# Performance work log

Measured on AMD Instinct MI355X. Metric: run time of the kernel, lower is better.

Reference implementation:

```python
import jax, jax.numpy as jnp
import numpy as np

H = 16        # query heads
HK = 8        # key/value heads
HD = 128      # head dim
EPS = 1e-6
THETA = 1000000.0


def _rmsnorm(x, w):
    # per-head RMSNorm over last dim (head_dim)
    var = jnp.mean(jnp.square(x.astype(jnp.float32)), axis=-1, keepdims=True)
    return (x * jax.lax.rsqrt(var + EPS)).astype(x.dtype) * w


def _rope(x, cos, sin):
    # x: [B, S, h, HD]; cos/sin: [S, HD//2]
    x1, x2 = jnp.split(x, 2, axis=-1)
    c = cos[None, :, None, :]
    s = sin[None, :, None, :]
    return jnp.concatenate([x1 * c - x2 * s, x2 * c + x1 * s], axis=-1)


def setup_inputs() -> dict:
    key = jax.random.key(0)
    ks = jax.random.split(key, 5)
    B, S, D = 2, 2048, 2048
    scale = 0.02
    return {
        "x": jax.random.normal(ks[0], (B, S, D), jnp.float32),
        "wq": jax.random.normal(ks[1], (H * HD, D), jnp.float32) * scale,
        "wk": jax.random.normal(ks[2], (HK * HD, D), jnp.float32) * scale,
        "wv": jax.random.normal(ks[3], (HK * HD, D), jnp.float32) * scale,
        "wo": jax.random.normal(ks[4], (D, H * HD), jnp.float32) * scale,
        "q_norm_w": jnp.ones((HD,), jnp.float32),
        "k_norm_w": jnp.ones((HD,), jnp.float32),
    }


def reference(x, wq, wk, wv, wo, q_norm_w, k_norm_w):
    B, S, D = x.shape
    # QKV projections (no bias)
    q = (x @ wq.T).reshape(B, S, H, HD)
    k = (x @ wk.T).reshape(B, S, HK, HD)
    v = (x @ wv.T).reshape(B, S, HK, HD)

    # per-head RMSNorm on Q and K (Qwen3 qk-norm)
    q = _rmsnorm(q, q_norm_w)
    k = _rmsnorm(k, k_norm_w)

    # RoPE
    inv_freq = 1.0 / (THETA ** (jnp.arange(0, HD, 2, dtype=jnp.float32) / HD))
    ang = jnp.arange(S, dtype=jnp.float32)[:, None] * inv_freq[None, :]  # [S, HD/2]
    cos, sin = jnp.cos(ang), jnp.sin(ang)
    q = _rope(q, cos, sin)
    k = _rope(k, cos, sin)

    # GQA: repeat KV heads to match query heads
    rep = H // HK
    k = jnp.repeat(k, rep, axis=2)  # [B, S, H, HD]
    v = jnp.repeat(v, rep, axis=2)

    # causal SDPA
    scores = jnp.einsum("bqhd,bkhd->bhqk", q, k) / jnp.sqrt(jnp.float32(HD))
    mask = jnp.tril(jnp.ones((S, S), dtype=bool))
    scores = jnp.where(mask[None, None], scores, jnp.finfo(scores.dtype).min)
    probs = jax.nn.softmax(scores, axis=-1)
    out = jnp.einsum("bhqk,bkhd->bqhd", probs, v).reshape(B, S, H * HD)

    return out @ wo.T
```

## Files before the change

kernel.cpp:

```cpp
#include <hip/hip_runtime.h>
#include <hip/hip_bf16.h>
#include <math.h>

#define B_   2
#define S_   2048
#define D_   2048
#define H_   16
#define HK_  8
#define HD_  128
#define BS_  (B_ * S_)
#define NQKV 4096
#define SCALE 0.08838834764831845f

typedef __bf16 bf16x8 __attribute__((ext_vector_type(8)));
typedef __bf16 bf16x4 __attribute__((ext_vector_type(4)));
typedef float  f32x4  __attribute__((ext_vector_type(4)));

#define AS1(p) ((const __attribute__((address_space(1))) void*)(p))
#define AS3(p) ((__attribute__((address_space(3))) void*)(p))

template <int S>
__device__ __forceinline__ float ror16(float x) {
    return __builtin_bit_cast(float, __builtin_amdgcn_update_dpp(
        0, __builtin_bit_cast(int, x), 0x120 | S, 0xF, 0xF, true));
}
__device__ __forceinline__ float row_sum16(float x) {
    x += ror16<8>(x);
    x += ror16<4>(x);
    x += ror16<2>(x);
    x += ror16<1>(x);
    return x;
}

__global__ __launch_bounds__(256) void cvt_all(const float* __restrict__ x,
                                               const float* __restrict__ wq,
                                               const float* __restrict__ wk,
                                               const float* __restrict__ wv,
                                               const float* __restrict__ wo,
                                               __bf16* __restrict__ xb,
                                               __bf16* __restrict__ wb,
                                               __bf16* __restrict__ wob) {
    int bid = blockIdx.x;
    const float* src;
    __bf16* dst;
    int i4;
    if (bid < 8192)       { src = x;  dst = xb;                    i4 = bid * 256; }
    else if (bid < 12288) { src = wq; dst = wb;                    i4 = (bid - 8192) * 256; }
    else if (bid < 14336) { src = wk; dst = wb + (size_t)4194304;  i4 = (bid - 12288) * 256; }
    else if (bid < 16384) { src = wv; dst = wb + (size_t)6291456;  i4 = (bid - 14336) * 256; }
    else                  { src = wo; dst = wob;                   i4 = (bid - 16384) * 256; }
    i4 += threadIdx.x;
    float4 v = reinterpret_cast<const float4*>(src)[i4];
    bf16x4 o = {(__bf16)v.x, (__bf16)v.y, (__bf16)v.z, (__bf16)v.w};
    reinterpret_cast<bf16x4*>(dst)[i4] = o;
}

__global__ __launch_bounds__(128) void build_rope(float* __restrict__ tab) {
    int s = blockIdx.x;
    int d = threadIdx.x;
    int i = d & 63;
    float inv_freq = exp2f(-19.931568569324174f * (float)(2 * i) * (1.0f / 128.0f));
    float ang = (float)s * inv_freq;
    float sn, cs;
    sincosf(ang, &sn, &cs);
    tab[s * 128 + d] = (d < 64) ? cs : sn;
}

__global__ __launch_bounds__(512, 2) void gemm_bf16_8ph(const __bf16* __restrict__ A,
                                                        const __bf16* __restrict__ W,
                                                        __bf16* __restrict__ C,
                                                        int M, int N, int K) {
    __shared__ __bf16 lds[2][2][256 * 64];

    const int t    = threadIdx.x;
    const int w    = t >> 6;
    const int lane = t & 63;
    const int col  = lane & 15;
    const int quad = lane >> 4;
    const int c7   = col & 7;
    const int wm   = w >> 2;
    const int wn   = w & 3;

    const int bid = blockIdx.x;
    const int nid = (bid & 7) * 32 + (bid >> 3);
    const int st  = nid >> 4;
    const int wi  = nid & 15;
    const int m0 = ((st >> 2) * 4 + (wi >> 2)) * 256;
    const int n0 = ((st & 3) * 4 + (wi & 3)) * 256;

    const int lr8 = lane >> 3;
    const int sw8 = ((lane & 7) ^ lr8) * 8;
    const __bf16* Ag = A + (size_t)(m0 + w * 16 + lr8) * K + sw8;
    const __bf16* Wg = W + (size_t)(n0 + w * 16 + lr8) * K + sw8;

    const int nkt = K >> 6;
    const int nit = nkt >> 1;

    const int aBase = (wm * 128 + col) * 64;
    const int bBase = (wn * 64 + col) * 64;
    const int kx0 = (quad ^ c7) * 8;
    const int kx1 = ((4 + quad) ^ c7) * 8;

    f32x4 acc[8][4];
    #pragma unroll
    for (int i = 0; i < 8; i++)
        #pragma unroll
        for (int j = 0; j < 4; j++) acc[i][j] = (f32x4){0.f, 0.f, 0.f, 0.f};

    bf16x8 a[4][2], a2[4][2], b0f[2][2], b1f[2][2];

    auto stg = [&](int ktv, int bufc, int ab, int half) {
        if (ktv >= nkt) return;
        const __bf16* gb = (ab ? Wg : Ag) + (size_t)half * 128 * K + (size_t)ktv * 64;
        __bf16* db = &lds[bufc][ab][(half * 128 + w * 16) * 64];
        __builtin_amdgcn_global_load_lds(AS1(gb), AS3(db), 16, 0, 0);
        __builtin_amdgcn_global_load_lds(AS1(gb + (size_t)8 * K), AS3(db + 512), 16, 0, 0);
    };
    auto lda = [&](bf16x8 (&dst)[4][2], const __bf16* panel, int g) {
        #pragma unroll
        for (int mi = 0; mi < 4; mi++) {
            dst[mi][0] = *reinterpret_cast<const bf16x8*>(&panel[aBase + (g * 64 + mi * 16) * 64 + kx0]);
            dst[mi][1] = *reinterpret_cast<const bf16x8*>(&panel[aBase + (g * 64 + mi * 16) * 64 + kx1]);
        }
    };
    auto ldb = [&](bf16x8 (&dst)[2][2], const __bf16* panel, int ng) {
        #pragma unroll
        for (int ni = 0; ni < 2; ni++) {
            dst[ni][0] = *reinterpret_cast<const bf16x8*>(&panel[bBase + (ng * 32 + ni * 16) * 64 + kx0]);
            dst[ni][1] = *reinterpret_cast<const bf16x8*>(&panel[bBase + (ng * 32 + ni * 16) * 64 + kx1]);
        }
    };
    auto mm = [&](bf16x8 (&af)[4][2], bf16x8 (&bfr)[2][2], int g, int ng) {
        __builtin_amdgcn_s_setprio(1);
        #pragma unroll
        for (int mi = 0; mi < 4; mi++)
            #pragma unroll
            for (int ni = 0; ni < 2; ni++) {
                f32x4 c = acc[g * 4 + mi][ng * 2 + ni];
                c = __builtin_amdgcn_mfma_f32_16x16x32_bf16(af[mi][0], bfr[ni][0], c, 0, 0, 0);
                c = __builtin_amdgcn_mfma_f32_16x16x32_bf16(af[mi][1], bfr[ni][1], c, 0, 0, 0);
                acc[g * 4 + mi][ng * 2 + ni] = c;
            }
        __builtin_amdgcn_s_setprio(0);
    };

#define BAR  __builtin_amdgcn_s_barrier()
#define LGKM0 do { asm volatile("s_waitcnt lgkmcnt(0)" ::: "memory"); \
                   __builtin_amdgcn_sched_barrier(0); } while (0)
#define VM(n) asm volatile("s_waitcnt vmcnt(" #n ")" ::: "memory")

    stg(0, 0, 0, 0); stg(0, 0, 0, 1); stg(0, 0, 1, 0); stg(0, 0, 1, 1);
    stg(1, 1, 0, 0); stg(1, 1, 0, 1);
    VM(4);
    BAR;

    #pragma unroll 1
    for (int it = 0; it < nit; ++it) {
        const int k2 = it * 2;
        const bool last = (it == nit - 1);

        const __bf16* A0p = &lds[0][0][0];
        const __bf16* B0p = &lds[0][1][0];
        const __bf16* A1p = &lds[1][0][0];
        const __bf16* B1p = &lds[1][1][0];

        lda(a, A0p, 0); ldb(b0f, B0p, 0);
        stg(k2 + 1, 1, 1, 0);
        BAR; LGKM0;
        mm(a, b0f, 0, 0);
        lda(a2, A0p, 1);
        stg(k2 + 1, 1, 1, 1);
        BAR; LGKM0;
        mm(a2, b0f, 1, 0);
        ldb(b1f, B0p, 1);
        stg(k2 + 2, 0, 0, 0);
        BAR; LGKM0;
        mm(a, b1f, 0, 1);
        stg(k2 + 2, 0, 0, 1);
        if (last) VM(0); else VM(4);
        BAR;
        mm(a2, b1f, 1, 1);

        lda(a, A1p, 0); ldb(b0f, B1p, 0);
        stg(k2 + 2, 0, 1, 0);
        BAR; LGKM0;
        mm(a, b0f, 0, 0);
        lda(a2, A1p, 1);
        stg(k2 + 2, 0, 1, 1);
        BAR; LGKM0;
        mm(a2, b0f, 1, 0);
        ldb(b1f, B1p, 1);
        stg(k2 + 3, 1, 0, 0);
        BAR; LGKM0;
        mm(a, b1f, 0, 1);
        stg(k2 + 3, 1, 0, 1);
        if (!last) { VM(4); }
        BAR;
        mm(a2, b1f, 1, 1);
    }

#undef BAR
#undef LGKM0
#undef VM

    #pragma unroll
    for (int m8 = 0; m8 < 8; m8++) {
        #pragma unroll
        for (int r = 0; r < 4; r++) {
            size_t row = m0 + wm * 128 + m8 * 16 + quad * 4 + r;
            __bf16* cp = C + row * N + n0 + wn * 64 + col;
            #pragma unroll
            for (int n4 = 0; n4 < 4; n4++) cp[n4 * 16] = (__bf16)acc[m8][n4][r];
        }
    }
}

template <typename CT>
__global__ __launch_bounds__(256) void gemm_bf16_nt(const __bf16* __restrict__ A,
                                                    const __bf16* __restrict__ W,
                                                    CT* __restrict__ C,
                                                    int M, int N, int K) {
    __shared__ __bf16 As[128 * 64];
    __shared__ __bf16 Bs[128 * 64];

    const int t    = threadIdx.x;
    const int w    = t >> 6;
    const int lane = t & 63;
    const int col  = lane & 15;
    const int quad = lane >> 4;
    const int wm   = w >> 1;
    const int wn   = w & 1;

    const int m0 = blockIdx.y * 128;
    const int n0 = blockIdx.x * 128;

    const int lrow8 = lane >> 3;
    const int lch   = ((lane & 7) ^ lrow8) * 8;

    const __bf16* agp = A + (size_t)(m0 + w * 32 + lrow8) * K + lch;
    const __bf16* wgp = W + (size_t)(n0 + w * 32 + lrow8) * K + lch;
    __bf16* alp = As + (w * 32) * 64;
    __bf16* blp = Bs + (w * 32) * 64;

    const int c7 = col & 7;

    f32x4 acc[4][4];
    #pragma unroll
    for (int m = 0; m < 4; m++)
        #pragma unroll
        for (int n = 0; n < 4; n++) acc[m][n] = (f32x4){0.f, 0.f, 0.f, 0.f};

    #pragma unroll 1
    for (int k0 = 0; k0 < K; k0 += 64) {
        #pragma unroll
        for (int j = 0; j < 4; j++) {
            __builtin_amdgcn_global_load_lds(AS1(agp + k0 + (size_t)(j * 8) * K),
                                             AS3(alp + j * 512), 16, 0, 0);
            __builtin_amdgcn_global_load_lds(AS1(wgp + k0 + (size_t)(j * 8) * K),
                                             AS3(blp + j * 512), 16, 0, 0);
        }
        __syncthreads();

        #pragma unroll
        for (int kk = 0; kk < 2; kk++) {
            bf16x8 af[4], bfr[4];
            #pragma unroll
            for (int m = 0; m < 4; m++)
                af[m] = *reinterpret_cast<const bf16x8*>(
                    &As[(wm * 64 + m * 16 + col) * 64 + ((kk * 4 + quad) ^ c7) * 8]);
            #pragma unroll
            for (int n = 0; n < 4; n++)
                bfr[n] = *reinterpret_cast<const bf16x8*>(
                    &Bs[(wn * 64 + n * 16 + col) * 64 + ((kk * 4 + quad) ^ c7) * 8]);

            #pragma unroll
            for (int m = 0; m < 4; m++)
                #pragma unroll
                for (int n = 0; n < 4; n++)
                    acc[m][n] = __builtin_amdgcn_mfma_f32_16x16x32_bf16(af[m], bfr[n], acc[m][n], 0, 0, 0);
        }
        __syncthreads();
    }

    #pragma unroll
    for (int m = 0; m < 4; m++) {
        #pragma unroll
        for (int r = 0; r < 4; r++) {
            size_t row = m0 + wm * 64 + m * 16 + quad * 4 + r;
            CT* cp = C + row * N + n0 + wn * 64 + col;
            #pragma unroll
            for (int n = 0; n < 4; n++) cp[n * 16] = (CT)acc[m][n][r];
        }
    }
}

__global__ __launch_bounds__(256) void norm_rope(__bf16* __restrict__ qkv,
                                                 const float* __restrict__ qw,
                                                 const float* __restrict__ kw,
                                                 const float* __restrict__ tab) {
    const int g    = blockIdx.x * 16 + (threadIdx.x >> 4);
    const int l    = threadIdx.x & 15;
    const int row  = g / 24;
    const int head = g - row * 24;
    const int s    = row & (S_ - 1);

    const float* w = (head < H_) ? qw : kw;
    __bf16* p = qkv + (size_t)row * NQKV + head * HD_ + l * 8;

    bf16x8 xv = *reinterpret_cast<const bf16x8*>(p);
    float xf[8];
    float ss = 0.f;
    #pragma unroll
    for (int j = 0; j < 8; j++) { xf[j] = (float)xv[j]; ss = fmaf(xf[j], xf[j], ss); }
    ss = row_sum16(ss);
    float rs = rsqrtf(ss * (1.0f / 128.0f) + 1e-6f);

    float nf[8];
    const float4 w0 = *reinterpret_cast<const float4*>(&w[l * 8]);
    const float4 w1 = *reinterpret_cast<const float4*>(&w[l * 8 + 4]);
    nf[0] = xf[0] * rs * w0.x; nf[1] = xf[1] * rs * w0.y;
    nf[2] = xf[2] * rs * w0.z; nf[3] = xf[3] * rs * w0.w;
    nf[4] = xf[4] * rs * w1.x; nf[5] = xf[5] * rs * w1.y;
    nf[6] = xf[6] * rs * w1.z; nf[7] = xf[7] * rs * w1.w;

    float of[8];
    #pragma unroll
    for (int j = 0; j < 8; j++) of[j] = __shfl_xor(nf[j], 8);

    const int ib = (l & 7) * 8;
    const float4 c0 = *reinterpret_cast<const float4*>(&tab[s * 128 + ib]);
    const float4 c1 = *reinterpret_cast<const float4*>(&tab[s * 128 + ib + 4]);
    const float4 s0 = *reinterpret_cast<const float4*>(&tab[s * 128 + 64 + ib]);
    const float4 s1 = *reinterpret_cast<const float4*>(&tab[s * 128 + 64 + ib + 4]);
    float cs[8] = {c0.x, c0.y, c0.z, c0.w, c1.x, c1.y, c1.z, c1.w};
    float sn[8] = {s0.x, s0.y, s0.z, s0.w, s1.x, s1.y, s1.z, s1.w};

    bf16x8 out;
    if (l < 8) {
        #pragma unroll
        for (int j = 0; j < 8; j++) out[j] = (__bf16)(nf[j] * cs[j] - of[j] * sn[j]);
    } else {
        #pragma unroll
        for (int j = 0; j < 8; j++) out[j] = (__bf16)(of[j] * sn[j] + nf[j] * cs[j]);
    }
    *reinterpret_cast<bf16x8*>(p) = out;
}

__global__ __launch_bounds__(256) void transpose_v(const __bf16* __restrict__ qkv,
                                                   __bf16* __restrict__ vt) {
    __shared__ __bf16 Ls[64][136];
    const int t  = threadIdx.x;
    const int bk = blockIdx.y;
    const int b  = bk >> 3;
    const int kvh = bk & 7;
    const int s0 = blockIdx.x * 64;

    #pragma unroll
    for (int i = 0; i < 4; i++) {
        int f = t + i * 256;
        int row = f >> 4;
        int d8 = (f & 15) * 8;
        bf16x8 v = *reinterpret_cast<const bf16x8*>(
            &qkv[(size_t)(b * S_ + s0 + row) * NQKV + 3072 + kvh * HD_ + d8]);
        *reinterpret_cast<bf16x8*>(&Ls[row][d8]) = v;
    }
    __syncthreads();

    #pragma unroll
    for (int i = 0; i < 4; i++) {
        int f = t + i * 256;
        int dim = f >> 3;
        int kc = f & 7;
        bf16x8 o;
        #pragma unroll
        for (int e = 0; e < 8; e++) o[e] = Ls[kc * 8 + e][dim];
        *reinterpret_cast<bf16x8*>(
            &vt[((size_t)bk * HD_ + dim) * S_ + s0 + kc * 8]) = o;
    }
}

__global__ __launch_bounds__(256) void attn_mfma(const __bf16* __restrict__ qkv,
                                                 const __bf16* __restrict__ vt,
                                                 __bf16* __restrict__ ao) {
    __shared__ __align__(16) char smem[17408];
    __bf16 (*Qs)[136] = reinterpret_cast<__bf16(*)[136]>(smem);
    __bf16 (*Ks)[136] = reinterpret_cast<__bf16(*)[136]>(smem);
    __shared__ __bf16 Vt[128][72];
    __shared__ __bf16 Ps[4][16][72];

    const int t    = threadIdx.x;
    const int w    = t >> 6;
    const int lane = t & 63;
    const int col  = lane & 15;
    const int quad = lane >> 4;

    const int bh  = blockIdx.x;
    const int b   = bh >> 4;
    const int h   = bh & 15;
    const int kvh = h >> 1;
    const int qb  = gridDim.y - 1 - blockIdx.y;
    const int r0  = qb * 64;

    const float C0 = SCALE * 1.44269504f;
    const float CM = -12.0f * 1.44269504f;

    const __bf16* vbase = vt + ((size_t)(b * HK_ + kvh) * HD_) * S_;

    const __bf16* kp[4];
    __bf16*       kw_[4];
    const __bf16* vp[4];
    __bf16*       vw_[4];
    #pragma unroll
    for (int i = 0; i < 4; i++) {
        int f = t + i * 256;
        int row = f >> 4, d8 = (f & 15) * 8;
        kp[i]  = qkv + (size_t)(b * S_ + row) * NQKV + 2048 + kvh * HD_ + d8;
        kw_[i] = &Ks[row][d8];
        int dim = f >> 3, kc = f & 7;
        vp[i]  = vbase + (size_t)dim * S_ + kc * 8;
        vw_[i] = &Vt[dim][kc * 8];
    }

    bf16x8 kreg[4], vreg[4];
    #pragma unroll
    for (int i = 0; i < 4; i++) {
        kreg[i] = *reinterpret_cast<const bf16x8*>(kp[i]);  kp[i] += (size_t)64 * NQKV;
        vreg[i] = *reinterpret_cast<const bf16x8*>(vp[i]);  vp[i] += 64;
    }

    #pragma unroll
    for (int i = 0; i < 4; i++) {
        int f   = t + i * 256;
        int row = f >> 4;
        int d8  = (f & 15) * 8;
        bf16x8 v = *reinterpret_cast<const bf16x8*>(
            &qkv[(size_t)(b * S_ + r0 + row) * NQKV + h * HD_ + d8]);
        *reinterpret_cast<bf16x8*>(&Qs[row][d8]) = v;
    }
    __syncthreads();

    bf16x8 qf[4];
    {
        const int m = w * 16 + col;
        #pragma unroll
        for (int k = 0; k < 4; k++)
            qf[k] = *reinterpret_cast<const bf16x8*>(&Qs[m][k * 32 + quad * 8]);
    }

    f32x4 o_acc[8];
    #pragma unroll
    for (int i = 0; i < 8; i++) o_acc[i] = (f32x4){0.f, 0.f, 0.f, 0.f};
    float l_lane[4] = {0.f, 0.f, 0.f, 0.f};

    const int ntiles = qb + 1;
    for (int ti = 0; ti < ntiles; ti++) {
        __syncthreads();

        #pragma unroll
        for (int i = 0; i < 4; i++) {
            *reinterpret_cast<bf16x8*>(kw_[i]) = kreg[i];
            *reinterpret_cast<bf16x8*>(vw_[i]) = vreg[i];
        }
        if (ti + 1 < ntiles) {
            #pragma unroll
            for (int i = 0; i < 4; i++) {
                kreg[i] = *reinterpret_cast<const bf16x8*>(kp[i]);  kp[i] += (size_t)64 * NQKV;
                vreg[i] = *reinterpret_cast<const bf16x8*>(vp[i]);  vp[i] += 64;
            }
        }
        __syncthreads();

        f32x4 s[4];
        #pragma unroll
        for (int n = 0; n < 4; n++) {
            f32x4 acc = (f32x4){0.f, 0.f, 0.f, 0.f};
            #pragma unroll
            for (int k = 0; k < 4; k++) {
                bf16x8 bf = *reinterpret_cast<const bf16x8*>(
                    &Ks[n * 16 + col][k * 32 + quad * 8]);
                acc = __builtin_amdgcn_mfma_f32_16x16x32_bf16(qf[k], bf, acc, 0, 0, 0);
            }
            s[n] = acc;
        }

        const bool diag = (ti == qb);
        #pragma unroll
        for (int r = 0; r < 4; r++) {
            float p0 = exp2f(fmaf(s[0][r], C0, CM));
            float p1 = exp2f(fmaf(s[1][r], C0, CM));
            float p2 = exp2f(fmaf(s[2][r], C0, CM));
            float p3 = exp2f(fmaf(s[3][r], C0, CM));
            if (diag) {
                int qloc = w * 16 + quad * 4 + r;
                if (0 * 16 + col > qloc) p0 = 0.f;
                if (1 * 16 + col > qloc) p1 = 0.f;
                if (2 * 16 + col > qloc) p2 = 0.f;
                if (3 * 16 + col > qloc) p3 = 0.f;
            }
            l_lane[r] += p0 + p1 + p2 + p3;
            Ps[w][quad * 4 + r][0 * 16 + col] = (__bf16)p0;
            Ps[w][quad * 4 + r][1 * 16 + col] = (__bf16)p1;
            Ps[w][quad * 4 + r][2 * 16 + col] = (__bf16)p2;
            Ps[w][quad * 4 + r][3 * 16 + col] = (__bf16)p3;
        }

        bf16x8 pf[2];
        #pragma unroll
        for (int ks = 0; ks < 2; ks++)
            pf[ks] = *reinterpret_cast<const bf16x8*>(&Ps[w][col][ks * 32 + quad * 8]);
        #pragma unroll
        for (int n = 0; n < 8; n++) {
            #pragma unroll
            for (int ks = 0; ks < 2; ks++) {
                bf16x8 vf = *reinterpret_cast<const bf16x8*>(
                    &Vt[n * 16 + col][ks * 32 + quad * 8]);
                o_acc[n] = __builtin_amdgcn_mfma_f32_16x16x32_bf16(pf[ks], vf, o_acc[n], 0, 0, 0);
            }
        }
    }

    #pragma unroll
    for (int r = 0; r < 4; r++) {
        float l = row_sum16(l_lane[r]);
        float inv = 1.0f / l;
        int qrow = r0 + w * 16 + quad * 4 + r;
        __bf16* op = ao + (size_t)(b * S_ + qrow) * (H_ * HD_) + h * HD_ + col;
        #pragma unroll
        for (int n = 0; n < 8; n++)
            op[n * 16] = (__bf16)(o_acc[n][r] * inv);
    }
}

extern "C" void kernel_launch(void* const* d_in, const int* in_sizes, int n_in,
                              void* d_out, int out_size, void* d_ws, size_t ws_size,
                              hipStream_t stream) {
    const float* x  = (const float*)d_in[0];
    const float* wq = (const float*)d_in[1];
    const float* wk = (const float*)d_in[2];
    const float* wv = (const float*)d_in[3];
    const float* wo = (const float*)d_in[4];
    const float* qw = (const float*)d_in[5];
    const float* kw = (const float*)d_in[6];
    float* out = (float*)d_out;

    __bf16* ws  = (__bf16*)d_ws;
    __bf16* xb  = ws;
    __bf16* wb  = xb  + (size_t)8388608;
    __bf16* wob = wb  + (size_t)8388608;
    __bf16* qkv = wob + (size_t)4194304;
    __bf16* ao  = qkv + (size_t)16777216;
    __bf16* vtg = ao  + (size_t)8388608;
    float* rtab = (float*)ao;

    cvt_all<<<20480, 256, 0, stream>>>(x, wq, wk, wv, wo, xb, wb, wob);
    build_rope<<<S_, 128, 0, stream>>>(rtab);

    gemm_bf16_8ph<<<256, 512, 0, stream>>>(xb, wb, qkv, BS_, NQKV, D_);

    norm_rope<<<(BS_ * 24) / 16, 256, 0, stream>>>(qkv, qw, kw, rtab);

    transpose_v<<<dim3(S_ / 64, B_ * HK_), 256, 0, stream>>>(qkv, vtg);

    attn_mfma<<<dim3(B_ * H_, S_ / 64), 256, 0, stream>>>(qkv, vtg, ao);

    gemm_bf16_nt<float><<<dim3(D_ / 128, BS_ / 128), 256, 0, stream>>>(
        ao, wob, out, BS_, D_, H_ * HD_);
}
```

Baseline: 327.7 us.

## Fuse rope table into cvt, V transpose into norm_rope, drop LDS waits

The RoPE table build moves into extra blocks of the conversion kernel, and the V transpose moves into extra blocks of the norm/rope kernel, which cuts two kernel launches. The explicit lgkmcnt(0) waits and sched_barriers after each barrier in the QKV GEMM are removed, leaving the compiler to insert LDS waits itself. Dropping the sched_barrier may let the compiler interleave MFMAs with LDS reads, but it could also change the schedule in unpredictable ways.

```diff
diff --git a/kernel.cpp b/kernel.cpp
--- a/kernel.cpp
+++ b/kernel.cpp
@@ -39,8 +39,21 @@
                                                const float* __restrict__ wo,
                                                __bf16* __restrict__ xb,
                                                __bf16* __restrict__ wb,
-                                               __bf16* __restrict__ wob) {
+                                               __bf16* __restrict__ wob,
+                                               float* __restrict__ rtab) {
     int bid = blockIdx.x;
+    if (bid >= 20480) {
+        int idx = bid - 20480;
+        int s = idx * 2 + (threadIdx.x >> 7);
+        int d = threadIdx.x & 127;
+        int i = d & 63;
+        float inv_freq = exp2f(-19.931568569324174f * (float)(2 * i) * (1.0f / 128.0f));
+        float ang = (float)s * inv_freq;
+        float sn, cs;
+        sincosf(ang, &sn, &cs);
+        rtab[s * 128 + d] = (d < 64) ? cs : sn;
+        return;
+    }
     const float* src;
     __bf16* dst;
     int i4;
@@ -55,17 +68,6 @@
     reinterpret_cast<bf16x4*>(dst)[i4] = o;
 }
 
-__global__ __launch_bounds__(128) void build_rope(float* __restrict__ tab) {
-    int s = blockIdx.x;
-    int d = threadIdx.x;
-    int i = d & 63;
-    float inv_freq = exp2f(-19.931568569324174f * (float)(2 * i) * (1.0f / 128.0f));
-    float ang = (float)s * inv_freq;
-    float sn, cs;
-    sincosf(ang, &sn, &cs);
-    tab[s * 128 + d] = (d < 64) ? cs : sn;
-}
-
 __global__ __launch_bounds__(512, 2) void gemm_bf16_8ph(const __bf16* __restrict__ A,
                                                         const __bf16* __restrict__ W,
                                                         __bf16* __restrict__ C,
@@ -145,8 +147,6 @@
     };
 
 #define BAR  __builtin_amdgcn_s_barrier()
-#define LGKM0 do { asm volatile("s_waitcnt lgkmcnt(0)" ::: "memory"); \
-                   __builtin_amdgcn_sched_barrier(0); } while (0)
 #define VM(n) asm volatile("s_waitcnt vmcnt(" #n ")" ::: "memory")
 
     stg(0, 0, 0, 0); stg(0, 0, 0, 1); stg(0, 0, 1, 0); stg(0, 0, 1, 1);
@@ -166,15 +166,15 @@
 
         lda(a, A0p, 0); ldb(b0f, B0p, 0);
         stg(k2 + 1, 1, 1, 0);
-        BAR; LGKM0;
+        BAR;
         mm(a, b0f, 0, 0);
         lda(a2, A0p, 1);
         stg(k2 + 1, 1, 1, 1);
-        BAR; LGKM0;
+        BAR;
         mm(a2, b0f, 1, 0);
         ldb(b1f, B0p, 1);
         stg(k2 + 2, 0, 0, 0);
-        BAR; LGKM0;
+        BAR;
         mm(a, b1f, 0, 1);
         stg(k2 + 2, 0, 0, 1);
         if (last) VM(0); else VM(4);
@@ -183,15 +183,15 @@
 
         lda(a, A1p, 0); ldb(b0f, B1p, 0);
         stg(k2 + 2, 0, 1, 0);
-        BAR; LGKM0;
+        BAR;
         mm(a, b0f, 0, 0);
         lda(a2, A1p, 1);
         stg(k2 + 2, 0, 1, 1);
-        BAR; LGKM0;
+        BAR;
         mm(a2, b0f, 1, 0);
         ldb(b1f, B1p, 1);
         stg(k2 + 3, 1, 0, 0);
-        BAR; LGKM0;
+        BAR;
         mm(a, b1f, 0, 1);
         stg(k2 + 3, 1, 0, 1);
         if (!last) { VM(4); }
@@ -200,7 +200,6 @@
     }
 
 #undef BAR
-#undef LGKM0
 #undef VM
 
     #pragma unroll
@@ -294,10 +293,45 @@
     }
 }
 
-__global__ __launch_bounds__(256) void norm_rope(__bf16* __restrict__ qkv,
-                                                 const float* __restrict__ qw,
-                                                 const float* __restrict__ kw,
-                                                 const float* __restrict__ tab) {
+__global__ __launch_bounds__(256) void norm_rope_tv(__bf16* __restrict__ qkv,
+                                                    const float* __restrict__ qw,
+                                                    const float* __restrict__ kw,
+                                                    const float* __restrict__ tab,
+                                                    __bf16* __restrict__ vt) {
+    if (blockIdx.x >= 6144) {
+        __shared__ __bf16 Ls[64][136];
+        const int t  = threadIdx.x;
+        const int idx = blockIdx.x - 6144;
+        const int bk = idx >> 5;
+        const int b  = bk >> 3;
+        const int kvh = bk & 7;
+        const int s0 = (idx & 31) * 64;
+
+        #pragma unroll
+        for (int i = 0; i < 4; i++) {
+            int f = t + i * 256;
+            int row = f >> 4;
+            int d8 = (f & 15) * 8;
+            bf16x8 v = *reinterpret_cast<const bf16x8*>(
+                &qkv[(size_t)(b * S_ + s0 + row) * NQKV + 3072 + kvh * HD_ + d8]);
+            *reinterpret_cast<bf16x8*>(&Ls[row][d8]) = v;
+        }
+        __syncthreads();
+
+        #pragma unroll
+        for (int i = 0; i < 4; i++) {
+            int f = t + i * 256;
+            int dim = f >> 3;
+            int kc = f & 7;
+            bf16x8 o;
+            #pragma unroll
+            for (int e = 0; e < 8; e++) o[e] = Ls[kc * 8 + e][dim];
+            *reinterpret_cast<bf16x8*>(
+                &vt[((size_t)bk * HD_ + dim) * S_ + s0 + kc * 8]) = o;
+        }
+        return;
+    }
+
     const int g    = blockIdx.x * 16 + (threadIdx.x >> 4);
     const int l    = threadIdx.x & 15;
     const int row  = g / 24;
@@ -344,39 +378,6 @@
         for (int j = 0; j < 8; j++) out[j] = (__bf16)(of[j] * sn[j] + nf[j] * cs[j]);
     }
     *reinterpret_cast<bf16x8*>(p) = out;
-}
-
-__global__ __launch_bounds__(256) void transpose_v(const __bf16* __restrict__ qkv,
-                                                   __bf16* __restrict__ vt) {
-    __shared__ __bf16 Ls[64][136];
-    const int t  = threadIdx.x;
-    const int bk = blockIdx.y;
-    const int b  = bk >> 3;
-    const int kvh = bk & 7;
-    const int s0 = blockIdx.x * 64;
-
-    #pragma unroll
-    for (int i = 0; i < 4; i++) {
-        int f = t + i * 256;
-        int row = f >> 4;
-        int d8 = (f & 15) * 8;
-        bf16x8 v = *reinterpret_cast<const bf16x8*>(
-            &qkv[(size_t)(b * S_ + s0 + row) * NQKV + 3072 + kvh * HD_ + d8]);
-        *reinterpret_cast<bf16x8*>(&Ls[row][d8]) = v;
-    }
-    __syncthreads();
-
-    #pragma unroll
-    for (int i = 0; i < 4; i++) {
-        int f = t + i * 256;
-        int dim = f >> 3;
-        int kc = f & 7;
-        bf16x8 o;
-        #pragma unroll
-        for (int e = 0; e < 8; e++) o[e] = Ls[kc * 8 + e][dim];
-        *reinterpret_cast<bf16x8*>(
-            &vt[((size_t)bk * HD_ + dim) * S_ + s0 + kc * 8]) = o;
-    }
 }
 
 __global__ __launch_bounds__(256) void attn_mfma(const __bf16* __restrict__ qkv,
@@ -552,14 +553,11 @@
     __bf16* vtg = ao  + (size_t)8388608;
     float* rtab = (float*)ao;
 
-    cvt_all<<<20480, 256, 0, stream>>>(x, wq, wk, wv, wo, xb, wb, wob);
-    build_rope<<<S_, 128, 0, stream>>>(rtab);
+    cvt_all<<<21504, 256, 0, stream>>>(x, wq, wk, wv, wo, xb, wb, wob, rtab);
 
     gemm_bf16_8ph<<<256, 512, 0, stream>>>(xb, wb, qkv, BS_, NQKV, D_);
 
-    norm_rope<<<(BS_ * 24) / 16, 256, 0, stream>>>(qkv, qw, kw, rtab);
-
-    transpose_v<<<dim3(S_ / 64, B_ * HK_), 256, 0, stream>>>(qkv, vtg);
+    norm_rope_tv<<<6656, 256, 0, stream>>>(qkv, qw, kw, rtab, vtg);
 
     attn_mfma<<<dim3(B_ * H_, S_ / 64), 256, 0, stream>>>(qkv, vtg, ao);
 
```

After: 325.4 us. No clear change (-0.7%).
